# Performance work log

Hardware: AMD Instinct MI355X
Metric: run time of the kernel (lower is better)

Reference implementation:

```python
import jax, jax.numpy as jnp
from jax import lax
import numpy as np

# TopoLoss(dim=1, p=2, topo_lambda=1.0)
# p=2 -> Euclidean ground metric for the Vietoris-Rips filtration.
# This reference computes the dominant H0 persistence diagram of the VR complex:
# for a point cloud, H0 births are all 0 and deaths are exactly the MST edge
# weights (Kruskal/union-find == Prim, computed here with a fixed-length scan).
# Wasserstein distance between the two diagrams (equal cardinality N-1, births 0)
# reduces to optimal 1D matching of the sorted death values (q=1, the
# torch_topological WassersteinDistance default).
TOPO_LAMBDA = 1.0
EPS = 1e-12


def _pairwise_euclidean(x):
    # x: [B, N, D] -> [B, N, N] via the Gram trick (avoids [B,N,N,D] temp)
    sq = jnp.sum(x * x, axis=-1)                      # [B, N]
    g = jnp.einsum('bnd,bmd->bnm', x, x)              # [B, N, N]
    d2 = sq[:, :, None] + sq[:, None, :] - 2.0 * g
    return jnp.sqrt(jnp.maximum(d2, 0.0) + EPS)


def _mst_deaths(D):
    # Prim's algorithm on a dense distance matrix D: [N, N].
    # Returns the sorted MST edge weights = H0 death times ([N-1]).
    N = D.shape[0]
    inf = jnp.asarray(jnp.inf, D.dtype)
    in_tree0 = jnp.zeros((N,), bool).at[0].set(True)
    min_dist0 = D[0]

    def step(carry, _):
        in_tree, min_dist = carry
        masked = jnp.where(in_tree, inf, min_dist)
        j = jnp.argmin(masked)
        death = masked[j]
        in_tree = in_tree.at[j].set(True)
        min_dist = jnp.minimum(min_dist, D[j])
        return (in_tree, min_dist), death

    _, deaths = lax.scan(step, (in_tree0, min_dist0), None, length=N - 1)
    return jnp.sort(deaths)


def _h0_diagram_deaths(x):
    # x: [B, N, D] -> sorted death values [B, N-1]
    D = _pairwise_euclidean(x)
    return jax.vmap(_mst_deaths)(D)


def setup_inputs() -> dict:
    key = jax.random.key(0)
    k1, k2 = jax.random.split(key)
    B, N, D = 64, 1024, 3
    gts = jax.random.normal(k1, (B, N, D), dtype=jnp.float32)
    preds = jax.random.normal(k2, (B, N, D), dtype=jnp.float32)
    return {"gts": gts, "preds": preds}


def reference(gts, preds):
    # note: source names pers_info_pred = complex(gts) (vars swapped there);
    # Wasserstein is symmetric so ordering is irrelevant.
    deaths_a = _h0_diagram_deaths(gts)    # [B, N-1]
    deaths_b = _h0_diagram_deaths(preds)  # [B, N-1]
    # W1 between diagrams with equal cardinality and births==0:
    # optimal matching of sorted death coordinates.
    per_batch = jnp.sum(jnp.abs(deaths_a - deaths_b), axis=-1)  # [B]
    return per_batch.mean() * TOPO_LAMBDA
```

## Files before the change

### kernel.cpp

```cpp
#include <hip/hip_runtime.h>
#include <math.h>

#define N 1024
#define T 1024
#define HALF 512
#define PHASE_CAP 10
#define SWITCH 80

typedef float v2f __attribute__((ext_vector_type(2)));
typedef unsigned long long ull;

#define INF64 0xFFFFFFFFFFFFFFFFull
#define INF32 0xFFFFFFFFu

__device__ __forceinline__ unsigned umin32(unsigned a, unsigned b) { return a < b ? a : b; }
__device__ __forceinline__ unsigned umax32(unsigned a, unsigned b) { return a > b ? a : b; }
__device__ __forceinline__ int imin32(int a, int b) { return a < b ? a : b; }

__device__ __forceinline__ unsigned walk_root(const unsigned* parent, unsigned x) {
    unsigned prev = x, cur = parent[x];
    while (cur != prev) {
        unsigned nxt = parent[cur];
        if (nxt == prev) { cur = umin32(cur, prev); break; }
        prev = cur; cur = nxt;
    }
    return cur;
}

#define DPP_MIN_SHR(v, sh)                                                                   \
    do {                                                                                     \
        unsigned _t = (unsigned)__builtin_amdgcn_update_dpp(                                 \
            (int)0xFFFFFFFF, (int)(v), 0x110 | (sh), 0xF, 0xF, false);                       \
        (v) = umin32((v), _t);                                                               \
    } while (0)

__global__ __launch_bounds__(T) void scan1_kernel(const float* __restrict__ gts,
                                                  const float* __restrict__ preds,
                                                  unsigned* __restrict__ bests1) {
    __shared__ float px[N], py[N], pz[N];
    __shared__ float stage[3 * N];
    __shared__ unsigned pb[2][HALF];
    const int t = threadIdx.x;
    const int cloud = blockIdx.x >> 1;
    const int nh = blockIdx.x & 1;
    const float* __restrict__ src = (cloud < 64 ? gts : preds) + (size_t)(cloud & 63) * N * 3;

    if (t < 768) ((float4*)stage)[t] = ((const float4*)src)[t];
    __syncthreads();
    px[t] = stage[3 * t]; py[t] = stage[3 * t + 1]; pz[t] = stage[3 * t + 2];
    __syncthreads();

    const int node = nh * HALF + (t & (HALF - 1));
    const int jb = (t >> 9) * HALF;
    const float ax = px[node], ay = py[node], az = pz[node];
    const v2f axv = (v2f){ax, ax}, ayv = (v2f){ay, ay}, azv = (v2f){az, az};
    unsigned best = INF32;
    #pragma unroll 8
    for (int jj = 0; jj < HALF; jj += 2) {
        int j = jb + jj;
        v2f qx = *(const v2f*)&px[j];
        v2f qy = *(const v2f*)&py[j];
        v2f qz = *(const v2f*)&pz[j];
        v2f dx = axv - qx, dy = ayv - qy, dz = azv - qz;
        v2f e = dx * dx;
        e = __builtin_elementwise_fma(dy, dy, e);
        e = __builtin_elementwise_fma(dz, dz, e);
        unsigned k0 = (__float_as_uint(e.x) & 0xFFFFF800u) | (unsigned)j;
        unsigned k1 = (__float_as_uint(e.y) & 0xFFFFF800u) | (unsigned)(j + 1);
        k0 = (j == node) ? INF32 : k0;
        k1 = (j + 1 == node) ? INF32 : k1;
        best = umin32(best, umin32(k0, k1));
    }
    pb[t >> 9][t & (HALF - 1)] = best;
    __syncthreads();
    if (t < HALF)
        bests1[(size_t)cloud * N + nh * HALF + t] = umin32(pb[0][t], pb[1][t]);
}

__global__ __launch_bounds__(T) void scan2_kernel(const float* __restrict__ gts,
                                                  const float* __restrict__ preds,
                                                  const unsigned* __restrict__ bests1,
                                                  unsigned* __restrict__ bests2) {
    __shared__ float px[N], py[N], pz[N];
    __shared__ float stage[3 * N];
    __shared__ unsigned cw[N];
    __shared__ unsigned parent[N];
    __shared__ unsigned pb[2][HALF];
    const int t = threadIdx.x;
    const int cloud = blockIdx.x >> 1;
    const int nh = blockIdx.x & 1;
    const float* __restrict__ src = (cloud < 64 ? gts : preds) + (size_t)(cloud & 63) * N * 3;

    if (t < 768) ((float4*)stage)[t] = ((const float4*)src)[t];
    __syncthreads();
    px[t] = stage[3 * t]; py[t] = stage[3 * t + 1]; pz[t] = stage[3 * t + 2];
    parent[t] = bests1[(size_t)cloud * N + t] & 0x3FFu;
    __syncthreads();
    {
        unsigned r = walk_root(parent, (unsigned)t);
        parent[t] = r;
        cw[t] = r;
    }
    __syncthreads();

    const int node = nh * HALF + (t & (HALF - 1));
    const int jb = (t >> 9) * HALF;
    const unsigned c0 = cw[node];
    const float ax = px[node], ay = py[node], az = pz[node];
    const v2f axv = (v2f){ax, ax}, ayv = (v2f){ay, ay}, azv = (v2f){az, az};
    unsigned best = INF32;
    #pragma unroll 8
    for (int jj = 0; jj < HALF; jj += 2) {
        int j = jb + jj;
        v2f qx = *(const v2f*)&px[j];
        v2f qy = *(const v2f*)&py[j];
        v2f qz = *(const v2f*)&pz[j];
        uint2 cj = *(const uint2*)&cw[j];
        v2f dx = axv - qx, dy = ayv - qy, dz = azv - qz;
        v2f e = dx * dx;
        e = __builtin_elementwise_fma(dy, dy, e);
        e = __builtin_elementwise_fma(dz, dz, e);
        unsigned k0 = (__float_as_uint(e.x) & 0xFFFFF800u) | (unsigned)j;
        unsigned k1 = (__float_as_uint(e.y) & 0xFFFFF800u) | (unsigned)(j + 1);
        k0 = (cj.x == c0) ? INF32 : k0;
        k1 = (cj.y == c0) ? INF32 : k1;
        best = umin32(best, umin32(k0, k1));
    }
    pb[t >> 9][t & (HALF - 1)] = best;
    __syncthreads();
    if (t < HALF)
        bests2[(size_t)cloud * N + nh * HALF + t] = umin32(pb[0][t], pb[1][t]);
}

__global__ __launch_bounds__(T) void final_kernel(const float* __restrict__ gts,
                                                  const float* __restrict__ preds,
                                                  float* __restrict__ ws,
                                                  const unsigned* __restrict__ bests1,
                                                  const unsigned* __restrict__ bests2,
                                                  int nPre) {
    __shared__ float4 pts[N];
    __shared__ float4 spts[N];
    __shared__ unsigned comp[N];
    __shared__ ull bestComp[N];
    __shared__ unsigned parent[N];
    __shared__ __align__(16) unsigned pb[2][N];
    __shared__ float deaths[N];
    __shared__ unsigned wsum[16];
    __shared__ int deathCount;

    const int t = threadIdx.x;
    const int blk = blockIdx.x;
    const float* __restrict__ src = (blk < 64 ? gts : preds) + (size_t)(blk & 63) * N * 3;

    {
        float* stg = (float*)&spts[0];
        if (t < 768) ((float4*)stg)[t] = ((const float4*)src)[t];
        __syncthreads();
        float x = stg[3 * t], y = stg[3 * t + 1], z = stg[3 * t + 2];
        pts[t] = make_float4(x, y, z, __uint_as_float((unsigned)t));
        comp[t] = (unsigned)t;
        parent[t] = (unsigned)t;
        deaths[t] = 0.0f;
        bestComp[t] = INF64;
    }
    if (t == 0) deathCount = 0;
    __syncthreads();

    const int n = t & (HALF - 1);
    const int h = t >> 9;
    const int n2 = n + HALF;
    const int jbase = h * HALF;
    float4 pA = pts[n], pB = pts[n2];
    const v2f pxv = (v2f){pA.x, pB.x};
    const v2f pyv = (v2f){pA.y, pB.y};
    const v2f pzv = (v2f){pA.z, pB.z};

    if (nPre >= 1) {
        unsigned b1 = bests1[(size_t)blk * N + t];
        unsigned j1 = b1 & 0x3FFu;
        unsigned e1 = b1 & 0xFFFFF800u;
        parent[t] = j1;
        __syncthreads();
        {
            unsigned p = j1;
            unsigned gp = parent[p];
            bool mutual = (gp == (unsigned)t);
            bool rec = !mutual || ((unsigned)t < p);
            float dval = rec ? sqrtf(__uint_as_float(e1) + 1e-12f) : 0.0f;
            ull m = __ballot(rec);
            int cnt = __popcll(m);
            int base = 0;
            if ((t & 63) == 0 && cnt) base = atomicAdd(&deathCount, cnt);
            base = __shfl(base, 0, 64);
            if (rec) {
                int idx = base + __popcll(m & ((1ull << (t & 63)) - 1ull));
                if (idx < N - 1) deaths[idx] = dval;
            }
        }
        __syncthreads();
        {
            unsigned r = walk_root(parent, (unsigned)t);
            parent[t] = r;
            comp[t] = r;
            pts[t].w = __uint_as_float(r);
        }
        __syncthreads();
    }

    if (nPre >= 2) {
        unsigned b2 = bests2[(size_t)blk * N + t];
        if (b2 != INF32) {
            unsigned j2 = b2 & 0x3FFu, e2 = b2 & 0xFFFFF800u;
            unsigned mn = umin32((unsigned)t, j2), mx = umax32((unsigned)t, j2);
            atomicMin(&bestComp[comp[t]], ((ull)e2 << 20) | (ull)((mn << 10) | mx));
        }
        __syncthreads();
        const unsigned c = (unsigned)t;
        const bool isRoot = (parent[c] == c);
        {
            ull bc = bestComp[c];
            if (isRoot && bc != INF64) {
                unsigned mn = (unsigned)((bc >> 10) & 0x3FFu);
                unsigned mx = (unsigned)(bc & 0x3FFu);
                unsigned cm = comp[mn];
                parent[c] = (cm == c) ? comp[mx] : cm;
            }
        }
        __syncthreads();
        {
            bool rec = false;
            float dval = 0.0f;
            unsigned p = parent[c];
            if (isRoot && p != c) {
                unsigned gp = parent[p];
                bool mutual = (gp == c);
                rec = !mutual || (c < p);
                if (rec) dval = sqrtf(__uint_as_float((unsigned)(bestComp[c] >> 20)) + 1e-12f);
            }
            ull m = __ballot(rec);
            int cnt = __popcll(m);
            int base = 0;
            if ((t & 63) == 0 && cnt) base = atomicAdd(&deathCount, cnt);
            base = __shfl(base, 0, 64);
            if (rec) {
                int idx = base + __popcll(m & ((1ull << (t & 63)) - 1ull));
                if (idx < N - 1) deaths[idx] = dval;
            }
        }
        __syncthreads();
        {
            unsigned r = walk_root(parent, c);
            parent[t] = r;
            unsigned nc = walk_root(parent, comp[t]);
            comp[t] = nc;
            pts[t].w = __uint_as_float(nc);
            bestComp[t] = INF64;
        }
        __syncthreads();
    }

    int phase = nPre;
    while (N - deathCount > SWITCH && phase < PHASE_CAP) {
        const unsigned c0 = comp[n], c1 = comp[n2];
        unsigned best0 = INF32, best1 = INF32;
        #pragma unroll 8
        for (int jj = 0; jj < HALF; ++jj) {
            int j = jbase + jj;
            float4 pj = pts[j];
            unsigned cj = __float_as_uint(pj.w);
            v2f dx = pxv - (v2f){pj.x, pj.x};
            v2f dy = pyv - (v2f){pj.y, pj.y};
            v2f dz = pzv - (v2f){pj.z, pj.z};
            v2f e = dx * dx;
            e = __builtin_elementwise_fma(dy, dy, e);
            e = __builtin_elementwise_fma(dz, dz, e);
            unsigned k0 = (__float_as_uint(e.x) & 0xFFFFF800u) | (unsigned)j;
            unsigned k1 = (__float_as_uint(e.y) & 0xFFFFF800u) | (unsigned)j;
            k0 = (cj == c0) ? INF32 : k0;
            k1 = (cj == c1) ? INF32 : k1;
            best0 = umin32(best0, k0);
            best1 = umin32(best1, k1);
        }
        pb[h][n] = best0;
        pb[h][n2] = best1;
        __syncthreads();
        if (h == 0) {
            #pragma unroll
            for (int s = 0; s < 2; ++s) {
                int m = s == 0 ? n : n2;
                unsigned fb = umin32(pb[0][m], pb[1][m]);
                if (fb != INF32) {
                    unsigned j = fb & 0x3FFu, e = fb & 0xFFFFF800u;
                    unsigned mn = umin32((unsigned)m, j), mx = umax32((unsigned)m, j);
                    ull key = ((ull)e << 20) | (ull)((mn << 10) | mx);
                    if (phase == 0) bestComp[m] = key;
                    else atomicMin(&bestComp[comp[m]], key);
                }
            }
        }
        __syncthreads();
        const unsigned c = (unsigned)t;
        const bool isRoot = (parent[c] == c);
        {
            ull bc = bestComp[c];
            if (isRoot && bc != INF64) {
                unsigned mn = (unsigned)((bc >> 10) & 0x3FFu);
                unsigned mx = (unsigned)(bc & 0x3FFu);
                unsigned cm = comp[mn];
                parent[c] = (cm == c) ? comp[mx] : cm;
            }
        }
        __syncthreads();
        {
            bool rec = false;
            float dval = 0.0f;
            unsigned p = parent[c];
            if (isRoot && p != c) {
                unsigned gp = parent[p];
                bool mutual = (gp == c);
                rec = !mutual || (c < p);
                if (rec) dval = sqrtf(__uint_as_float((unsigned)(bestComp[c] >> 20)) + 1e-12f);
            }
            ull m = __ballot(rec);
            int cnt = __popcll(m);
            int base = 0;
            if ((t & 63) == 0 && cnt) base = atomicAdd(&deathCount, cnt);
            base = __shfl(base, 0, 64);
            if (rec) {
                int idx = base + __popcll(m & ((1ull << (t & 63)) - 1ull));
                if (idx < N - 1) deaths[idx] = dval;
            }
        }
        __syncthreads();
        {
            unsigned r = walk_root(parent, c);
            parent[t] = r;
            unsigned nc = walk_root(parent, comp[t]);
            comp[t] = nc;
            pts[t].w = __uint_as_float(nc);
            bestComp[t] = INF64;
        }
        __syncthreads();
        ++phase;
    }

    const int dcbase = deathCount;
    const int comps = N - dcbase;
    if (comps > 1) {
        unsigned* scomp = &pb[0][0];
        unsigned* hist = &pb[1][0];
        unsigned* wavemin = &pb[1][0];
        uint2* segs = (uint2*)&bestComp[0];
        const int lane = t & 63;
        const int wid = t >> 6;

        hist[t] = 0;
        __syncthreads();
        atomicAdd(&hist[comp[t]], 1u);
        __syncthreads();
        unsigned cnt = hist[t];
        unsigned inc = cnt;
        #pragma unroll
        for (int d = 1; d < 64; d <<= 1) {
            unsigned u = __shfl_up(inc, d, 64);
            if (lane >= d) inc += u;
        }
        if (lane == 63) wsum[wid] = inc;
        __syncthreads();
        unsigned wof = 0;
        for (int i = 0; i < wid; ++i) wof += wsum[i];
        unsigned excl = wof + inc - cnt;
        if (cnt) { segs[t].x = excl; segs[t].y = excl + cnt; }
        __syncthreads();
        hist[t] = excl;
        __syncthreads();
        {
            unsigned pos = atomicAdd(&hist[comp[t]], 1u);
            spts[pos] = pts[t];
            scomp[pos] = comp[t];
        }
        __syncthreads();

        unsigned c_cur = comp[0];
        v2f pxv2 = (v2f){0.f, 0.f}, pyv2 = pxv2, pzv2 = pxv2;
        unsigned myc0 = 0, myc1 = 0, md0 = INF32, md1 = INF32;
        if (t < HALF) {
            float4 q0 = spts[t], q1 = spts[t + HALF];
            myc0 = scomp[t];
            myc1 = scomp[t + HALF];
            pxv2 = (v2f){q0.x, q1.x};
            pyv2 = (v2f){q0.y, q1.y};
            pzv2 = (v2f){q0.z, q1.z};
            if (myc0 == c_cur) pxv2.x = INFINITY;
            if (myc1 == c_cur) pxv2.y = INFINITY;
        }

        for (int step = 0; step < comps - 1; ++step) {
            if (t < HALF) {
                uint2 sg = segs[c_cur];
                const int jb = (int)sg.x, je = (int)sg.y, jl = je - 1;
                for (int base = jb; base < je; base += 4) {
                    float4 q0 = spts[base];
                    float4 q1 = spts[imin32(base + 1, jl)];
                    float4 q2 = spts[imin32(base + 2, jl)];
                    float4 q3 = spts[imin32(base + 3, jl)];
                    #define RELAX(qq)                                                        \
                        {                                                                    \
                            v2f dx = pxv2 - (v2f){qq.x, qq.x};                               \
                            v2f dy = pyv2 - (v2f){qq.y, qq.y};                               \
                            v2f dz = pzv2 - (v2f){qq.z, qq.z};                               \
                            v2f e = dx * dx;                                                 \
                            e = __builtin_elementwise_fma(dy, dy, e);                        \
                            e = __builtin_elementwise_fma(dz, dz, e);                        \
                            md0 = umin32(md0, (__float_as_uint(e.x) & 0xFFFFFC00u) | myc0);  \
                            md1 = umin32(md1, (__float_as_uint(e.y) & 0xFFFFFC00u) | myc1);  \
                        }
                    RELAX(q0) RELAX(q1) RELAX(q2) RELAX(q3)
                    #undef RELAX
                }
                unsigned v = umin32(md0, md1);
                DPP_MIN_SHR(v, 1);
                DPP_MIN_SHR(v, 2);
                DPP_MIN_SHR(v, 4);
                DPP_MIN_SHR(v, 8);
                unsigned r0 = (unsigned)__builtin_amdgcn_readlane((int)v, 15);
                unsigned r1 = (unsigned)__builtin_amdgcn_readlane((int)v, 31);
                unsigned r2 = (unsigned)__builtin_amdgcn_readlane((int)v, 47);
                unsigned r3 = (unsigned)__builtin_amdgcn_readlane((int)v, 63);
                if (lane == 0)
                    wavemin[(step & 1) * 8 + wid] = umin32(umin32(r0, r1), umin32(r2, r3));
            }
            __syncthreads();
            if (t < HALF) {
                const uint4* wmv = (const uint4*)(wavemin + (step & 1) * 8);
                uint4 u0 = wmv[0], u1 = wmv[1];
                unsigned m0 = umin32(umin32(u0.x, u0.y), umin32(u0.z, u0.w));
                unsigned m1 = umin32(umin32(u1.x, u1.y), umin32(u1.z, u1.w));
                unsigned G = umin32(m0, m1);
                c_cur = G & 0x3FFu;
                if (t == 0)
                    deaths[dcbase + step] = sqrtf(__uint_as_float(G & 0xFFFFFC00u) + 1e-12f);
                if (myc0 == c_cur) { pxv2.x = INFINITY; md0 = INF32; }
                if (myc1 == c_cur) { pxv2.y = INFINITY; md1 = INF32; }
            }
        }
    }

    if (t == 0) deaths[N - 1] = INFINITY;
    __syncthreads();
    {
        float v = deaths[t];
        #pragma unroll
        for (int k = 2; k <= N; k <<= 1) {
            const bool up = ((t & k) == 0);
            #pragma unroll
            for (int j = k >> 1; j > 0; j >>= 1) {
                float u;
                if (j >= 64) {
                    deaths[t] = v;
                    __syncthreads();
                    u = deaths[t ^ j];
                    __syncthreads();
                } else {
                    u = __shfl_xor(v, j, 64);
                }
                v = (((t & j) == 0) == up) ? fminf(v, u) : fmaxf(v, u);
            }
        }
        float* dst = ws + (size_t)blk * N;
        dst[t] = (t < N - 1) ? v : 0.0f;
    }
}

__global__ __launch_bounds__(256) void diff_kernel(const float* __restrict__ ws,
                                                   float* __restrict__ out) {
    __shared__ float red[4];
    const int t = threadIdx.x;
    const int b = blockIdx.x;
    const float* a = ws + (size_t)b * N;
    const float* c = ws + (size_t)(64 + b) * N;
    float sum = 0.0f;
    for (int i = t; i < N; i += 256)
        sum += fabsf(a[i] - c[i]);
    #pragma unroll
    for (int off = 32; off > 0; off >>= 1)
        sum += __shfl_down(sum, off, 64);
    if ((t & 63) == 0) red[t >> 6] = sum;
    __syncthreads();
    if (t == 0)
        atomicAdd(out, (red[0] + red[1] + red[2] + red[3]) * (1.0f / 64.0f));
}

extern "C" void kernel_launch(void* const* d_in, const int* in_sizes, int n_in,
                              void* d_out, int out_size, void* d_ws, size_t ws_size,
                              hipStream_t stream) {
    const float* gts = (const float*)d_in[0];
    const float* preds = (const float*)d_in[1];
    float* ws = (float*)d_ws;
    unsigned* bests1 = (unsigned*)d_ws;
    unsigned* bests2 = bests1 + 128 * N;
    const bool big = ws_size >= (size_t)(2u * 128u * N * 4u);

    if (big) {
        hipLaunchKernelGGL(scan1_kernel, dim3(256), dim3(T), 0, stream, gts, preds, bests1);
        hipLaunchKernelGGL(scan2_kernel, dim3(256), dim3(T), 0, stream, gts, preds, bests1, bests2);
        hipLaunchKernelGGL(final_kernel, dim3(128), dim3(T), 0, stream,
                           gts, preds, ws, bests1, bests2, 2);
    } else {
        hipLaunchKernelGGL(final_kernel, dim3(128), dim3(T), 0, stream,
                           gts, preds, ws, (const unsigned*)nullptr, (const unsigned*)nullptr, 0);
    }
    hipMemsetAsync(d_out, 0, sizeof(float), stream);
    hipLaunchKernelGGL(diff_kernel, dim3(64), dim3(256), 0, stream, ws, (float*)d_out);
}
```

Measured before the change: 223.3 us.

## Register-block four query nodes per thread in Boruvka scan kernels

Each thread in scan1 and scan2 now handles four query nodes packed into two v2f registers and sweeps a 128-candidate slice, instead of one node over 512 candidates. Every candidate point loaded from LDS is reused against four nodes, cutting shared-memory loads per distance, and the partial minima are reduced across eight slices instead of two. In exchange it uses more registers and a slightly larger final reduction.

```diff
diff --git a/kernel.cpp b/kernel.cpp
--- a/kernel.cpp
+++ b/kernel.cpp
@@ -39,7 +39,7 @@
                                                   unsigned* __restrict__ bests1) {
     __shared__ float px[N], py[N], pz[N];
     __shared__ float stage[3 * N];
-    __shared__ unsigned pb[2][HALF];
+    __shared__ unsigned pb8[8][HALF];
     const int t = threadIdx.x;
     const int cloud = blockIdx.x >> 1;
     const int nh = blockIdx.x & 1;
@@ -50,31 +50,52 @@
     px[t] = stage[3 * t]; py[t] = stage[3 * t + 1]; pz[t] = stage[3 * t + 2];
     __syncthreads();
 
-    const int node = nh * HALF + (t & (HALF - 1));
-    const int jb = (t >> 9) * HALF;
-    const float ax = px[node], ay = py[node], az = pz[node];
-    const v2f axv = (v2f){ax, ax}, ayv = (v2f){ay, ay}, azv = (v2f){az, az};
-    unsigned best = INF32;
-    #pragma unroll 8
-    for (int jj = 0; jj < HALF; jj += 2) {
-        int j = jb + jj;
+    const int q = t & 127;
+    const int s = t >> 7;
+    const int jbase = s << 7;
+    const int n0 = nh * HALF + q;
+    const int n1 = n0 + 128, n2 = n0 + 256, n3 = n0 + 384;
+    const v2f axA = (v2f){px[n0], px[n1]}, ayA = (v2f){py[n0], py[n1]}, azA = (v2f){pz[n0], pz[n1]};
+    const v2f axB = (v2f){px[n2], px[n3]}, ayB = (v2f){py[n2], py[n3]}, azB = (v2f){pz[n2], pz[n3]};
+    unsigned b0 = INF32, b1 = INF32, b2 = INF32, b3 = INF32;
+    #pragma unroll 4
+    for (int jj = 0; jj < 128; jj += 2) {
+        const int j = jbase + jj;
         v2f qx = *(const v2f*)&px[j];
         v2f qy = *(const v2f*)&py[j];
         v2f qz = *(const v2f*)&pz[j];
-        v2f dx = axv - qx, dy = ayv - qy, dz = azv - qz;
-        v2f e = dx * dx;
-        e = __builtin_elementwise_fma(dy, dy, e);
-        e = __builtin_elementwise_fma(dz, dz, e);
-        unsigned k0 = (__float_as_uint(e.x) & 0xFFFFF800u) | (unsigned)j;
-        unsigned k1 = (__float_as_uint(e.y) & 0xFFFFF800u) | (unsigned)(j + 1);
-        k0 = (j == node) ? INF32 : k0;
-        k1 = (j + 1 == node) ? INF32 : k1;
-        best = umin32(best, umin32(k0, k1));
-    }
-    pb[t >> 9][t & (HALF - 1)] = best;
-    __syncthreads();
-    if (t < HALF)
-        bests1[(size_t)cloud * N + nh * HALF + t] = umin32(pb[0][t], pb[1][t]);
+        #define STEP1(SX, SY, SZ, JV)                                                   \
+        {                                                                               \
+            const v2f sxv = (v2f){SX, SX}, syv = (v2f){SY, SY}, szv = (v2f){SZ, SZ};    \
+            v2f dxA = axA - sxv, dyA = ayA - syv, dzA = azA - szv;                      \
+            v2f eA = dxA * dxA;                                                         \
+            eA = __builtin_elementwise_fma(dyA, dyA, eA);                               \
+            eA = __builtin_elementwise_fma(dzA, dzA, eA);                               \
+            v2f dxB = axB - sxv, dyB = ayB - syv, dzB = azB - szv;                      \
+            v2f eB = dxB * dxB;                                                         \
+            eB = __builtin_elementwise_fma(dyB, dyB, eB);                               \
+            eB = __builtin_elementwise_fma(dzB, dzB, eB);                               \
+            unsigned kk;                                                                \
+            kk = (__float_as_uint(eA.x) & 0xFFFFF800u) | (unsigned)(JV);                \
+            b0 = umin32(b0, ((JV) == n0) ? INF32 : kk);                                 \
+            kk = (__float_as_uint(eA.y) & 0xFFFFF800u) | (unsigned)(JV);                \
+            b1 = umin32(b1, ((JV) == n1) ? INF32 : kk);                                 \
+            kk = (__float_as_uint(eB.x) & 0xFFFFF800u) | (unsigned)(JV);                \
+            b2 = umin32(b2, ((JV) == n2) ? INF32 : kk);                                 \
+            kk = (__float_as_uint(eB.y) & 0xFFFFF800u) | (unsigned)(JV);                \
+            b3 = umin32(b3, ((JV) == n3) ? INF32 : kk);                                 \
+        }
+        STEP1(qx.x, qy.x, qz.x, j)
+        STEP1(qx.y, qy.y, qz.y, j + 1)
+        #undef STEP1
+    }
+    pb8[s][q] = b0; pb8[s][q + 128] = b1; pb8[s][q + 256] = b2; pb8[s][q + 384] = b3;
+    __syncthreads();
+    if (t < HALF) {
+        unsigned best = umin32(umin32(pb8[0][t], pb8[1][t]), umin32(pb8[2][t], pb8[3][t]));
+        best = umin32(best, umin32(umin32(pb8[4][t], pb8[5][t]), umin32(pb8[6][t], pb8[7][t])));
+        bests1[(size_t)cloud * N + nh * HALF + t] = best;
+    }
 }
 
 __global__ __launch_bounds__(T) void scan2_kernel(const float* __restrict__ gts,
@@ -85,7 +106,7 @@
     __shared__ float stage[3 * N];
     __shared__ unsigned cw[N];
     __shared__ unsigned parent[N];
-    __shared__ unsigned pb[2][HALF];
+    __shared__ unsigned pb8[8][HALF];
     const int t = threadIdx.x;
     const int cloud = blockIdx.x >> 1;
     const int nh = blockIdx.x & 1;
@@ -103,33 +124,54 @@
     }
     __syncthreads();
 
-    const int node = nh * HALF + (t & (HALF - 1));
-    const int jb = (t >> 9) * HALF;
-    const unsigned c0 = cw[node];
-    const float ax = px[node], ay = py[node], az = pz[node];
-    const v2f axv = (v2f){ax, ax}, ayv = (v2f){ay, ay}, azv = (v2f){az, az};
-    unsigned best = INF32;
-    #pragma unroll 8
-    for (int jj = 0; jj < HALF; jj += 2) {
-        int j = jb + jj;
+    const int q = t & 127;
+    const int s = t >> 7;
+    const int jbase = s << 7;
+    const int n0 = nh * HALF + q;
+    const int n1 = n0 + 128, n2 = n0 + 256, n3 = n0 + 384;
+    const unsigned c0 = cw[n0], c1 = cw[n1], c2 = cw[n2], c3 = cw[n3];
+    const v2f axA = (v2f){px[n0], px[n1]}, ayA = (v2f){py[n0], py[n1]}, azA = (v2f){pz[n0], pz[n1]};
+    const v2f axB = (v2f){px[n2], px[n3]}, ayB = (v2f){py[n2], py[n3]}, azB = (v2f){pz[n2], pz[n3]};
+    unsigned b0 = INF32, b1 = INF32, b2 = INF32, b3 = INF32;
+    #pragma unroll 4
+    for (int jj = 0; jj < 128; jj += 2) {
+        const int j = jbase + jj;
         v2f qx = *(const v2f*)&px[j];
         v2f qy = *(const v2f*)&py[j];
         v2f qz = *(const v2f*)&pz[j];
         uint2 cj = *(const uint2*)&cw[j];
-        v2f dx = axv - qx, dy = ayv - qy, dz = azv - qz;
-        v2f e = dx * dx;
-        e = __builtin_elementwise_fma(dy, dy, e);
-        e = __builtin_elementwise_fma(dz, dz, e);
-        unsigned k0 = (__float_as_uint(e.x) & 0xFFFFF800u) | (unsigned)j;
-        unsigned k1 = (__float_as_uint(e.y) & 0xFFFFF800u) | (unsigned)(j + 1);
-        k0 = (cj.x == c0) ? INF32 : k0;
-        k1 = (cj.y == c0) ? INF32 : k1;
-        best = umin32(best, umin32(k0, k1));
-    }
-    pb[t >> 9][t & (HALF - 1)] = best;
-    __syncthreads();
-    if (t < HALF)
-        bests2[(size_t)cloud * N + nh * HALF + t] = umin32(pb[0][t], pb[1][t]);
+        #define STEP2(SX, SY, SZ, CJ, JV)                                               \
+        {                                                                               \
+            const v2f sxv = (v2f){SX, SX}, syv = (v2f){SY, SY}, szv = (v2f){SZ, SZ};    \
+            v2f dxA = axA - sxv, dyA = ayA - syv, dzA = azA - szv;                      \
+            v2f eA = dxA * dxA;                                                         \
+            eA = __builtin_elementwise_fma(dyA, dyA, eA);                               \
+            eA = __builtin_elementwise_fma(dzA, dzA, eA);                               \
+            v2f dxB = axB - sxv, dyB = ayB - syv, dzB = azB - szv;                      \
+            v2f eB = dxB * dxB;                                                         \
+            eB = __builtin_elementwise_fma(dyB, dyB, eB);                               \
+            eB = __builtin_elementwise_fma(dzB, dzB, eB);                               \
+            unsigned kk;                                                                \
+            kk = (__float_as_uint(eA.x) & 0xFFFFF800u) | (unsigned)(JV);                \
+            b0 = umin32(b0, ((CJ) == c0) ? INF32 : kk);                                 \
+            kk = (__float_as_uint(eA.y) & 0xFFFFF800u) | (unsigned)(JV);                \
+            b1 = umin32(b1, ((CJ) == c1) ? INF32 : kk);                                 \
+            kk = (__float_as_uint(eB.x) & 0xFFFFF800u) | (unsigned)(JV);                \
+            b2 = umin32(b2, ((CJ) == c2) ? INF32 : kk);                                 \
+            kk = (__float_as_uint(eB.y) & 0xFFFFF800u) | (unsigned)(JV);                \
+            b3 = umin32(b3, ((CJ) == c3) ? INF32 : kk);                                 \
+        }
+        STEP2(qx.x, qy.x, qz.x, cj.x, j)
+        STEP2(qx.y, qy.y, qz.y, cj.y, j + 1)
+        #undef STEP2
+    }
+    pb8[s][q] = b0; pb8[s][q + 128] = b1; pb8[s][q + 256] = b2; pb8[s][q + 384] = b3;
+    __syncthreads();
+    if (t < HALF) {
+        unsigned best = umin32(umin32(pb8[0][t], pb8[1][t]), umin32(pb8[2][t], pb8[3][t]));
+        best = umin32(best, umin32(umin32(pb8[4][t], pb8[5][t]), umin32(pb8[6][t], pb8[7][t])));
+        bests2[(size_t)cloud * N + nh * HALF + t] = best;
+    }
 }
 
 __global__ __launch_bounds__(T) void final_kernel(const float* __restrict__ gts,
```

Result: no change. 219.4 us (-1.7%).

## Fuse scan passes, Boruvka phases and final reduction into one mega kernel

Applied to the files above, without the earlier changes.

Replaces the separate scan1, scan2 and final kernels with a single per-cloud mega_kernel. The two nearest-neighbour scan passes are done in shared memory by one 1024-thread block per cloud instead of being split over two blocks through global workspace. The diff stage appears to be folded in with a ticket counter, so the last block writes the output. This removes launch overhead and global round trips, but halves the number of blocks doing the scan work, which costs parallelism in the heavy first phases.

```diff
diff --git a/kernel.cpp b/kernel.cpp
--- a/kernel.cpp
+++ b/kernel.cpp
@@ -34,110 +34,452 @@
         (v) = umin32((v), _t);                                                               \
     } while (0)
 
-__global__ __launch_bounds__(T) void scan1_kernel(const float* __restrict__ gts,
-                                                  const float* __restrict__ preds,
-                                                  unsigned* __restrict__ bests1) {
-    __shared__ float px[N], py[N], pz[N];
-    __shared__ float stage[3 * N];
-    __shared__ unsigned pb[2][HALF];
+struct MegaSmem {
+    float4 pts[N];
+    float deaths[N];
+    ull bestComp[N];
+    unsigned comp[N];
+    unsigned pb[2][N];
+    union {
+        struct {
+            unsigned pb4hi[2][N];
+            unsigned bests[N];
+            unsigned parent[N];
+        } a;
+        float4 spts[N];
+        float stage[3 * N];
+    } u;
+    unsigned wsum[16];
+    int deathCount;
+    int ticket;
+    float red4[2][4][4];
+};
+
+template <bool SUPP_COMP>
+__device__ __forceinline__ void scan_pass(MegaSmem& S, int t) {
+    const int q = t & 255;
+    const int s = t >> 8;
+    const int jbase = s << 8;
+    const int n0 = q, n1 = q + 256, n2 = q + 512, n3 = q + 768;
+    const float4 p0 = S.pts[n0], p1 = S.pts[n1], p2 = S.pts[n2], p3 = S.pts[n3];
+    const v2f axA = (v2f){p0.x, p1.x}, ayA = (v2f){p0.y, p1.y}, azA = (v2f){p0.z, p1.z};
+    const v2f axB = (v2f){p2.x, p3.x}, ayB = (v2f){p2.y, p3.y}, azB = (v2f){p2.z, p3.z};
+    unsigned c0 = 0, c1 = 0, c2 = 0, c3 = 0;
+    if (SUPP_COMP) { c0 = S.comp[n0]; c1 = S.comp[n1]; c2 = S.comp[n2]; c3 = S.comp[n3]; }
+    unsigned b0 = INF32, b1 = INF32, b2 = INF32, b3 = INF32;
+    #pragma unroll 4
+    for (int jj = 0; jj < 256; jj += 2) {
+        const int j = jbase + jj;
+        const float4 qa = S.pts[j];
+        const float4 qb = S.pts[j + 1];
+        uint2 cj;
+        if (SUPP_COMP) cj = *(const uint2*)&S.comp[j];
+        #define MSTEP(QQ, CJV, JV)                                                       \
+        {                                                                                \
+            const v2f sxv = (v2f){QQ.x, QQ.x}, syv = (v2f){QQ.y, QQ.y},                  \
+                      szv = (v2f){QQ.z, QQ.z};                                           \
+            v2f dxA = axA - sxv, dyA = ayA - syv, dzA = azA - szv;                       \
+            v2f eA = dxA * dxA;                                                          \
+            eA = __builtin_elementwise_fma(dyA, dyA, eA);                                \
+            eA = __builtin_elementwise_fma(dzA, dzA, eA);                                \
+            v2f dxB = axB - sxv, dyB = ayB - syv, dzB = azB - szv;                       \
+            v2f eB = dxB * dxB;                                                          \
+            eB = __builtin_elementwise_fma(dyB, dyB, eB);                                \
+            eB = __builtin_elementwise_fma(dzB, dzB, eB);                                \
+            unsigned kk;                                                                 \
+            kk = (__float_as_uint(eA.x) & 0xFFFFF800u) | (unsigned)(JV);                 \
+            b0 = umin32(b0, (SUPP_COMP ? ((CJV) == c0) : ((JV) == n0)) ? INF32 : kk);    \
+            kk = (__float_as_uint(eA.y) & 0xFFFFF800u) | (unsigned)(JV);                 \
+            b1 = umin32(b1, (SUPP_COMP ? ((CJV) == c1) : ((JV) == n1)) ? INF32 : kk);    \
+            kk = (__float_as_uint(eB.x) & 0xFFFFF800u) | (unsigned)(JV);                 \
+            b2 = umin32(b2, (SUPP_COMP ? ((CJV) == c2) : ((JV) == n2)) ? INF32 : kk);    \
+            kk = (__float_as_uint(eB.y) & 0xFFFFF800u) | (unsigned)(JV);                 \
+            b3 = umin32(b3, (SUPP_COMP ? ((CJV) == c3) : ((JV) == n3)) ? INF32 : kk);    \
+        }
+        MSTEP(qa, cj.x, j)
+        MSTEP(qb, cj.y, j + 1)
+        #undef MSTEP
+    }
+    unsigned* prow = (s < 2) ? &S.pb[s][0] : &S.u.a.pb4hi[s - 2][0];
+    prow[n0] = b0; prow[n1] = b1; prow[n2] = b2; prow[n3] = b3;
+    __syncthreads();
+    {
+        unsigned best = umin32(umin32(S.pb[0][t], S.pb[1][t]),
+                               umin32(S.u.a.pb4hi[0][t], S.u.a.pb4hi[1][t]));
+        S.u.a.bests[t] = best;
+    }
+    __syncthreads();
+}
+
+__global__ __launch_bounds__(T) void mega_kernel(const float* __restrict__ gts,
+                                                 const float* __restrict__ preds,
+                                                 float* __restrict__ ws,
+                                                 float* __restrict__ out,
+                                                 unsigned* __restrict__ ctr) {
+    __shared__ MegaSmem S;
     const int t = threadIdx.x;
-    const int cloud = blockIdx.x >> 1;
-    const int nh = blockIdx.x & 1;
-    const float* __restrict__ src = (cloud < 64 ? gts : preds) + (size_t)(cloud & 63) * N * 3;
-
-    if (t < 768) ((float4*)stage)[t] = ((const float4*)src)[t];
-    __syncthreads();
-    px[t] = stage[3 * t]; py[t] = stage[3 * t + 1]; pz[t] = stage[3 * t + 2];
-    __syncthreads();
-
-    const int node = nh * HALF + (t & (HALF - 1));
-    const int jb = (t >> 9) * HALF;
-    const float ax = px[node], ay = py[node], az = pz[node];
-    const v2f axv = (v2f){ax, ax}, ayv = (v2f){ay, ay}, azv = (v2f){az, az};
-    unsigned best = INF32;
-    #pragma unroll 8
-    for (int jj = 0; jj < HALF; jj += 2) {
-        int j = jb + jj;
-        v2f qx = *(const v2f*)&px[j];
-        v2f qy = *(const v2f*)&py[j];
-        v2f qz = *(const v2f*)&pz[j];
-        v2f dx = axv - qx, dy = ayv - qy, dz = azv - qz;
-        v2f e = dx * dx;
-        e = __builtin_elementwise_fma(dy, dy, e);
-        e = __builtin_elementwise_fma(dz, dz, e);
-        unsigned k0 = (__float_as_uint(e.x) & 0xFFFFF800u) | (unsigned)j;
-        unsigned k1 = (__float_as_uint(e.y) & 0xFFFFF800u) | (unsigned)(j + 1);
-        k0 = (j == node) ? INF32 : k0;
-        k1 = (j + 1 == node) ? INF32 : k1;
-        best = umin32(best, umin32(k0, k1));
-    }
-    pb[t >> 9][t & (HALF - 1)] = best;
-    __syncthreads();
-    if (t < HALF)
-        bests1[(size_t)cloud * N + nh * HALF + t] = umin32(pb[0][t], pb[1][t]);
-}
-
-__global__ __launch_bounds__(T) void scan2_kernel(const float* __restrict__ gts,
-                                                  const float* __restrict__ preds,
-                                                  const unsigned* __restrict__ bests1,
-                                                  unsigned* __restrict__ bests2) {
-    __shared__ float px[N], py[N], pz[N];
-    __shared__ float stage[3 * N];
-    __shared__ unsigned cw[N];
-    __shared__ unsigned parent[N];
-    __shared__ unsigned pb[2][HALF];
-    const int t = threadIdx.x;
-    const int cloud = blockIdx.x >> 1;
-    const int nh = blockIdx.x & 1;
-    const float* __restrict__ src = (cloud < 64 ? gts : preds) + (size_t)(cloud & 63) * N * 3;
-
-    if (t < 768) ((float4*)stage)[t] = ((const float4*)src)[t];
-    __syncthreads();
-    px[t] = stage[3 * t]; py[t] = stage[3 * t + 1]; pz[t] = stage[3 * t + 2];
-    parent[t] = bests1[(size_t)cloud * N + t] & 0x3FFu;
-    __syncthreads();
-    {
-        unsigned r = walk_root(parent, (unsigned)t);
-        parent[t] = r;
-        cw[t] = r;
-    }
-    __syncthreads();
-
-    const int node = nh * HALF + (t & (HALF - 1));
-    const int jb = (t >> 9) * HALF;
-    const unsigned c0 = cw[node];
-    const float ax = px[node], ay = py[node], az = pz[node];
-    const v2f axv = (v2f){ax, ax}, ayv = (v2f){ay, ay}, azv = (v2f){az, az};
-    unsigned best = INF32;
-    #pragma unroll 8
-    for (int jj = 0; jj < HALF; jj += 2) {
-        int j = jb + jj;
-        v2f qx = *(const v2f*)&px[j];
-        v2f qy = *(const v2f*)&py[j];
-        v2f qz = *(const v2f*)&pz[j];
-        uint2 cj = *(const uint2*)&cw[j];
-        v2f dx = axv - qx, dy = ayv - qy, dz = azv - qz;
-        v2f e = dx * dx;
-        e = __builtin_elementwise_fma(dy, dy, e);
-        e = __builtin_elementwise_fma(dz, dz, e);
-        unsigned k0 = (__float_as_uint(e.x) & 0xFFFFF800u) | (unsigned)j;
-        unsigned k1 = (__float_as_uint(e.y) & 0xFFFFF800u) | (unsigned)(j + 1);
-        k0 = (cj.x == c0) ? INF32 : k0;
-        k1 = (cj.y == c0) ? INF32 : k1;
-        best = umin32(best, umin32(k0, k1));
-    }
-    pb[t >> 9][t & (HALF - 1)] = best;
-    __syncthreads();
-    if (t < HALF)
-        bests2[(size_t)cloud * N + nh * HALF + t] = umin32(pb[0][t], pb[1][t]);
+    const int blk = blockIdx.x;
+    const float* __restrict__ src = (blk < 64 ? gts : preds) + (size_t)(blk & 63) * N * 3;
+
+    if (t < 768) ((float4*)S.u.stage)[t] = ((const float4*)src)[t];
+    __syncthreads();
+    {
+        const float x = S.u.stage[3 * t], y = S.u.stage[3 * t + 1], z = S.u.stage[3 * t + 2];
+        __syncthreads();
+        S.pts[t] = make_float4(x, y, z, __uint_as_float((unsigned)t));
+        S.comp[t] = (unsigned)t;
+        S.u.a.parent[t] = (unsigned)t;
+        S.deaths[t] = 0.0f;
+        S.bestComp[t] = INF64;
+        if (t == 0) S.deathCount = 0;
+    }
+    __syncthreads();
+
+    scan_pass<false>(S, t);
+
+    {
+        unsigned b1v = S.u.a.bests[t];
+        unsigned j1 = b1v & 0x3FFu;
+        unsigned e1 = b1v & 0xFFFFF800u;
+        S.u.a.parent[t] = j1;
+        __syncthreads();
+        {
+            unsigned p = j1;
+            unsigned gp = S.u.a.parent[p];
+            bool mutual = (gp == (unsigned)t);
+            bool rec = !mutual || ((unsigned)t < p);
+            float dval = rec ? sqrtf(__uint_as_float(e1) + 1e-12f) : 0.0f;
+            ull m = __ballot(rec);
+            int cnt = __popcll(m);
+            int base = 0;
+            if ((t & 63) == 0 && cnt) base = atomicAdd(&S.deathCount, cnt);
+            base = __shfl(base, 0, 64);
+            if (rec) {
+                int idx = base + __popcll(m & ((1ull << (t & 63)) - 1ull));
+                if (idx < N - 1) S.deaths[idx] = dval;
+            }
+        }
+        __syncthreads();
+        {
+            unsigned r = walk_root(S.u.a.parent, (unsigned)t);
+            S.u.a.parent[t] = r;
+            S.comp[t] = r;
+            S.pts[t].w = __uint_as_float(r);
+        }
+        __syncthreads();
+    }
+
+    scan_pass<true>(S, t);
+
+    {
+        unsigned b2v = S.u.a.bests[t];
+        if (b2v != INF32) {
+            unsigned j2 = b2v & 0x3FFu, e2 = b2v & 0xFFFFF800u;
+            unsigned mn = umin32((unsigned)t, j2), mx = umax32((unsigned)t, j2);
+            atomicMin(&S.bestComp[S.comp[t]], ((ull)e2 << 20) | (ull)((mn << 10) | mx));
+        }
+        __syncthreads();
+        const unsigned c = (unsigned)t;
+        const bool isRoot = (S.u.a.parent[c] == c);
+        {
+            ull bc = S.bestComp[c];
+            if (isRoot && bc != INF64) {
+                unsigned mn = (unsigned)((bc >> 10) & 0x3FFu);
+                unsigned mx = (unsigned)(bc & 0x3FFu);
+                unsigned cm = S.comp[mn];
+                S.u.a.parent[c] = (cm == c) ? S.comp[mx] : cm;
+            }
+        }
+        __syncthreads();
+        {
+            bool rec = false;
+            float dval = 0.0f;
+            unsigned p = S.u.a.parent[c];
+            if (isRoot && p != c) {
+                unsigned gp = S.u.a.parent[p];
+                bool mutual = (gp == c);
+                rec = !mutual || (c < p);
+                if (rec) dval = sqrtf(__uint_as_float((unsigned)(S.bestComp[c] >> 20)) + 1e-12f);
+            }
+            ull m = __ballot(rec);
+            int cnt = __popcll(m);
+            int base = 0;
+            if ((t & 63) == 0 && cnt) base = atomicAdd(&S.deathCount, cnt);
+            base = __shfl(base, 0, 64);
+            if (rec) {
+                int idx = base + __popcll(m & ((1ull << (t & 63)) - 1ull));
+                if (idx < N - 1) S.deaths[idx] = dval;
+            }
+        }
+        __syncthreads();
+        {
+            unsigned r = walk_root(S.u.a.parent, c);
+            S.u.a.parent[t] = r;
+            unsigned nc = walk_root(S.u.a.parent, S.comp[t]);
+            S.comp[t] = nc;
+            S.pts[t].w = __uint_as_float(nc);
+            S.bestComp[t] = INF64;
+        }
+        __syncthreads();
+    }
+
+    {
+        const int n = t & (HALF - 1);
+        const int h = t >> 9;
+        const int n2 = n + HALF;
+        const int jb2 = h * HALF;
+        float4 pA = S.pts[n], pB = S.pts[n2];
+        const v2f pxv = (v2f){pA.x, pB.x};
+        const v2f pyv = (v2f){pA.y, pB.y};
+        const v2f pzv = (v2f){pA.z, pB.z};
+        int phase = 2;
+        while (N - S.deathCount > SWITCH && phase < PHASE_CAP) {
+            const unsigned c0 = S.comp[n], c1 = S.comp[n2];
+            unsigned best0 = INF32, best1 = INF32;
+            #pragma unroll 8
+            for (int jj = 0; jj < HALF; ++jj) {
+                int j = jb2 + jj;
+                float4 pj = S.pts[j];
+                unsigned cj = __float_as_uint(pj.w);
+                v2f dx = pxv - (v2f){pj.x, pj.x};
+                v2f dy = pyv - (v2f){pj.y, pj.y};
+                v2f dz = pzv - (v2f){pj.z, pj.z};
+                v2f e = dx * dx;
+                e = __builtin_elementwise_fma(dy, dy, e);
+                e = __builtin_elementwise_fma(dz, dz, e);
+                unsigned k0 = (__float_as_uint(e.x) & 0xFFFFF800u) | (unsigned)j;
+                unsigned k1 = (__float_as_uint(e.y) & 0xFFFFF800u) | (unsigned)j;
+                k0 = (cj == c0) ? INF32 : k0;
+                k1 = (cj == c1) ? INF32 : k1;
+                best0 = umin32(best0, k0);
+                best1 = umin32(best1, k1);
+            }
+            S.pb[h][n] = best0;
+            S.pb[h][n2] = best1;
+            __syncthreads();
+            if (h == 0) {
+                #pragma unroll
+                for (int sS = 0; sS < 2; ++sS) {
+                    int m = sS == 0 ? n : n2;
+                    unsigned fb = umin32(S.pb[0][m], S.pb[1][m]);
+                    if (fb != INF32) {
+                        unsigned j = fb & 0x3FFu, e = fb & 0xFFFFF800u;
+                        unsigned mn = umin32((unsigned)m, j), mx = umax32((unsigned)m, j);
+                        ull key = ((ull)e << 20) | (ull)((mn << 10) | mx);
+                        atomicMin(&S.bestComp[S.comp[m]], key);
+                    }
+                }
+            }
+            __syncthreads();
+            const unsigned c = (unsigned)t;
+            const bool isRoot = (S.u.a.parent[c] == c);
+            {
+                ull bc = S.bestComp[c];
+                if (isRoot && bc != INF64) {
+                    unsigned mn = (unsigned)((bc >> 10) & 0x3FFu);
+                    unsigned mx = (unsigned)(bc & 0x3FFu);
+                    unsigned cm = S.comp[mn];
+                    S.u.a.parent[c] = (cm == c) ? S.comp[mx] : cm;
+                }
+            }
+            __syncthreads();
+            {
+                bool rec = false;
+                float dval = 0.0f;
+                unsigned p = S.u.a.parent[c];
+                if (isRoot && p != c) {
+                    unsigned gp = S.u.a.parent[p];
+                    bool mutual = (gp == c);
+                    rec = !mutual || (c < p);
+                    if (rec)
+                        dval = sqrtf(__uint_as_float((unsigned)(S.bestComp[c] >> 20)) + 1e-12f);
+                }
+                ull m = __ballot(rec);
+                int cnt = __popcll(m);
+                int base = 0;
+                if ((t & 63) == 0 && cnt) base = atomicAdd(&S.deathCount, cnt);
+                base = __shfl(base, 0, 64);
+                if (rec) {
+                    int idx = base + __popcll(m & ((1ull << (t & 63)) - 1ull));
+                    if (idx < N - 1) S.deaths[idx] = dval;
+                }
+            }
+            __syncthreads();
+            {
+                unsigned r = walk_root(S.u.a.parent, c);
+                S.u.a.parent[t] = r;
+                unsigned nc = walk_root(S.u.a.parent, S.comp[t]);
+                S.comp[t] = nc;
+                S.pts[t].w = __uint_as_float(nc);
+                S.bestComp[t] = INF64;
+            }
+            __syncthreads();
+            ++phase;
+        }
+    }
+
+    const int dcbase = S.deathCount;
+    const int comps = N - dcbase;
+    if (comps > 1) {
+        unsigned* scomp = &S.pb[0][0];
+        unsigned* hist = &S.pb[1][0];
+        unsigned* wavemin = &S.pb[1][0];
+        uint2* segs = (uint2*)&S.bestComp[0];
+        const int lane = t & 63;
+        const int wid = t >> 6;
+
+        hist[t] = 0;
+        __syncthreads();
+        atomicAdd(&hist[S.comp[t]], 1u);
+        __syncthreads();
+        unsigned cnt = hist[t];
+        unsigned inc = cnt;
+        #pragma unroll
+        for (int d = 1; d < 64; d <<= 1) {
+            unsigned uu = __shfl_up(inc, d, 64);
+            if (lane >= d) inc += uu;
+        }
+        if (lane == 63) S.wsum[wid] = inc;
+        __syncthreads();
+        unsigned wof = 0;
+        for (int i = 0; i < wid; ++i) wof += S.wsum[i];
+        unsigned excl = wof + inc - cnt;
+        if (cnt) { segs[t].x = excl; segs[t].y = excl + cnt; }
+        __syncthreads();
+        hist[t] = excl;
+        __syncthreads();
+        {
+            unsigned pos = atomicAdd(&hist[S.comp[t]], 1u);
+            S.u.spts[pos] = S.pts[t];
+            scomp[pos] = S.comp[t];
+        }
+        __syncthreads();
+
+        unsigned c_cur = S.comp[0];
+        v2f pxv2 = (v2f){0.f, 0.f}, pyv2 = pxv2, pzv2 = pxv2;
+        unsigned myc0 = 0, myc1 = 0, md0 = INF32, md1 = INF32;
+        if (t < HALF) {
+            float4 q0 = S.u.spts[t], q1 = S.u.spts[t + HALF];
+            myc0 = scomp[t];
+            myc1 = scomp[t + HALF];
+            pxv2 = (v2f){q0.x, q1.x};
+            pyv2 = (v2f){q0.y, q1.y};
+            pzv2 = (v2f){q0.z, q1.z};
+            if (myc0 == c_cur) pxv2.x = INFINITY;
+            if (myc1 == c_cur) pxv2.y = INFINITY;
+        }
+
+        for (int step = 0; step < comps - 1; ++step) {
+            if (t < HALF) {
+                uint2 sg = segs[c_cur];
+                const int jb = (int)sg.x, je = (int)sg.y, jl = je - 1;
+                for (int base = jb; base < je; base += 4) {
+                    float4 q0 = S.u.spts[base];
+                    float4 q1 = S.u.spts[imin32(base + 1, jl)];
+                    float4 q2 = S.u.spts[imin32(base + 2, jl)];
+                    float4 q3 = S.u.spts[imin32(base + 3, jl)];
+                    #define RELAX(qq)                                                        \
+                        {                                                                    \
+                            v2f dx = pxv2 - (v2f){qq.x, qq.x};                               \
+                            v2f dy = pyv2 - (v2f){qq.y, qq.y};                               \
+                            v2f dz = pzv2 - (v2f){qq.z, qq.z};                               \
+                            v2f e = dx * dx;                                                 \
+                            e = __builtin_elementwise_fma(dy, dy, e);                        \
+                            e = __builtin_elementwise_fma(dz, dz, e);                        \
+                            md0 = umin32(md0, (__float_as_uint(e.x) & 0xFFFFFC00u) | myc0);  \
+                            md1 = umin32(md1, (__float_as_uint(e.y) & 0xFFFFFC00u) | myc1);  \
+                        }
+                    RELAX(q0) RELAX(q1) RELAX(q2) RELAX(q3)
+                    #undef RELAX
+                }
+                unsigned v = umin32(md0, md1);
+                DPP_MIN_SHR(v, 1);
+                DPP_MIN_SHR(v, 2);
+                DPP_MIN_SHR(v, 4);
+                DPP_MIN_SHR(v, 8);
+                unsigned r0 = (unsigned)__builtin_amdgcn_readlane((int)v, 15);
+                unsigned r1 = (unsigned)__builtin_amdgcn_readlane((int)v, 31);
+                unsigned r2 = (unsigned)__builtin_amdgcn_readlane((int)v, 47);
+                unsigned r3 = (unsigned)__builtin_amdgcn_readlane((int)v, 63);
+                if (lane == 0)
+                    wavemin[(step & 1) * 8 + wid] = umin32(umin32(r0, r1), umin32(r2, r3));
+            }
+            __syncthreads();
+            if (t < HALF) {
+                const uint4* wmv = (const uint4*)(wavemin + (step & 1) * 8);
+                uint4 u0 = wmv[0], u1 = wmv[1];
+                unsigned m0 = umin32(umin32(u0.x, u0.y), umin32(u0.z, u0.w));
+                unsigned m1 = umin32(umin32(u1.x, u1.y), umin32(u1.z, u1.w));
+                unsigned G = umin32(m0, m1);
+                c_cur = G & 0x3FFu;
+                if (t == 0)
+                    S.deaths[dcbase + step] = sqrtf(__uint_as_float(G & 0xFFFFFC00u) + 1e-12f);
+                if (myc0 == c_cur) { pxv2.x = INFINITY; md0 = INF32; }
+                if (myc1 == c_cur) { pxv2.y = INFINITY; md1 = INF32; }
+            }
+        }
+    }
+
+    if (t == 0) S.deaths[N - 1] = INFINITY;
+    __syncthreads();
+    {
+        float v = S.deaths[t];
+        #pragma unroll
+        for (int k = 2; k <= N; k <<= 1) {
+            const bool up = ((t & k) == 0);
+            #pragma unroll
+            for (int j = k >> 1; j > 0; j >>= 1) {
+                float uu;
+                if (j >= 64) {
+                    S.deaths[t] = v;
+                    __syncthreads();
+                    uu = S.deaths[t ^ j];
+                    __syncthreads();
+                } else {
+                    uu = __shfl_xor(v, j, 64);
+                }
+                v = (((t & j) == 0) == up) ? fminf(v, uu) : fmaxf(v, uu);
+            }
+        }
+        float* dst = ws + (size_t)blk * N;
+        dst[t] = (t < N - 1) ? v : 0.0f;
+    }
+
+    __threadfence();
+    __syncthreads();
+    if (t == 0) S.ticket = (int)atomicAdd(ctr, 1u);
+    __syncthreads();
+    if (S.ticket == 127) {
+        __threadfence();
+        const int g = t >> 8, tl = t & 255;
+        float acc = 0.0f;
+        for (int chunk = 0; chunk < 16; ++chunk) {
+            const int b = (chunk << 2) + g;
+            const float* a = ws + (size_t)b * N;
+            const float* c = ws + (size_t)(64 + b) * N;
+            float sum = 0.0f;
+            for (int i = tl; i < N; i += 256)
+                sum += fabsf(a[i] - c[i]);
+            #pragma unroll
+            for (int off = 32; off > 0; off >>= 1)
+                sum += __shfl_down(sum, off, 64);
+            if ((tl & 63) == 0) S.red4[chunk & 1][g][tl >> 6] = sum;
+            __syncthreads();
+            if (t == 0) {
+                #pragma unroll
+                for (int gg = 0; gg < 4; ++gg) {
+                    const float* r = S.red4[chunk & 1][gg];
+                    acc += (r[0] + r[1] + r[2] + r[3]) * (1.0f / 64.0f);
+                }
+            }
+        }
+        if (t == 0) out[0] = acc;
+    }
 }
 
 __global__ __launch_bounds__(T) void final_kernel(const float* __restrict__ gts,
                                                   const float* __restrict__ preds,
-                                                  float* __restrict__ ws,
-                                                  const unsigned* __restrict__ bests1,
-                                                  const unsigned* __restrict__ bests2,
-                                                  int nPre) {
+                                                  float* __restrict__ ws) {
     __shared__ float4 pts[N];
     __shared__ float4 spts[N];
     __shared__ unsigned comp[N];
@@ -175,92 +517,8 @@
     const v2f pyv = (v2f){pA.y, pB.y};
     const v2f pzv = (v2f){pA.z, pB.z};
 
-    if (nPre >= 1) {
-        unsigned b1 = bests1[(size_t)blk * N + t];
-        unsigned j1 = b1 & 0x3FFu;
-        unsigned e1 = b1 & 0xFFFFF800u;
-        parent[t] = j1;
-        __syncthreads();
-        {
-            unsigned p = j1;
-            unsigned gp = parent[p];
-            bool mutual = (gp == (unsigned)t);
-            bool rec = !mutual || ((unsigned)t < p);
-            float dval = rec ? sqrtf(__uint_as_float(e1) + 1e-12f) : 0.0f;
-            ull m = __ballot(rec);
-            int cnt = __popcll(m);
-            int base = 0;
-            if ((t & 63) == 0 && cnt) base = atomicAdd(&deathCount, cnt);
-            base = __shfl(base, 0, 64);
-            if (rec) {
-                int idx = base + __popcll(m & ((1ull << (t & 63)) - 1ull));
-                if (idx < N - 1) deaths[idx] = dval;
-            }
-        }
-        __syncthreads();
-        {
-            unsigned r = walk_root(parent, (unsigned)t);
-            parent[t] = r;
-            comp[t] = r;
-            pts[t].w = __uint_as_float(r);
-        }
-        __syncthreads();
-    }
-
-    if (nPre >= 2) {
-        unsigned b2 = bests2[(size_t)blk * N + t];
-        if (b2 != INF32) {
-            unsigned j2 = b2 & 0x3FFu, e2 = b2 & 0xFFFFF800u;
-            unsigned mn = umin32((unsigned)t, j2), mx = umax32((unsigned)t, j2);
-            atomicMin(&bestComp[comp[t]], ((ull)e2 << 20) | (ull)((mn << 10) | mx));
-        }
-        __syncthreads();
-        const unsigned c = (unsigned)t;
-        const bool isRoot = (parent[c] == c);
-        {
-            ull bc = bestComp[c];
-            if (isRoot && bc != INF64) {
-                unsigned mn = (unsigned)((bc >> 10) & 0x3FFu);
-                unsigned mx = (unsigned)(bc & 0x3FFu);
-                unsigned cm = comp[mn];
-                parent[c] = (cm == c) ? comp[mx] : cm;
-            }
-        }
-        __syncthreads();
-        {
-            bool rec = false;
-            float dval = 0.0f;
-            unsigned p = parent[c];
-            if (isRoot && p != c) {
-                unsigned gp = parent[p];
-                bool mutual = (gp == c);
-                rec = !mutual || (c < p);
-                if (rec) dval = sqrtf(__uint_as_float((unsigned)(bestComp[c] >> 20)) + 1e-12f);
-            }
-            ull m = __ballot(rec);
-            int cnt = __popcll(m);
-            int base = 0;
-            if ((t & 63) == 0 && cnt) base = atomicAdd(&deathCount, cnt);
-            base = __shfl(base, 0, 64);
-            if (rec) {
-                int idx = base + __popcll(m & ((1ull << (t & 63)) - 1ull));
-                if (idx < N - 1) deaths[idx] = dval;
-            }
-        }
-        __syncthreads();
-        {
-            unsigned r = walk_root(parent, c);
-            parent[t] = r;
-            unsigned nc = walk_root(parent, comp[t]);
-            comp[t] = nc;
-            pts[t].w = __uint_as_float(nc);
-            bestComp[t] = INF64;
-        }
-        __syncthreads();
-    }
-
-    int phase = nPre;
-    while (N - deathCount > SWITCH && phase < PHASE_CAP) {
+    int phase = 0;
+    while (N - deathCount > 1 && phase < PHASE_CAP) {
         const unsigned c0 = comp[n], c1 = comp[n2];
         unsigned best0 = INF32, best1 = INF32;
         #pragma unroll 8
@@ -344,108 +602,6 @@
         ++phase;
     }
 
-    const int dcbase = deathCount;
-    const int comps = N - dcbase;
-    if (comps > 1) {
-        unsigned* scomp = &pb[0][0];
-        unsigned* hist = &pb[1][0];
-        unsigned* wavemin = &pb[1][0];
-        uint2* segs = (uint2*)&bestComp[0];
-        const int lane = t & 63;
-        const int wid = t >> 6;
-
-        hist[t] = 0;
-        __syncthreads();
-        atomicAdd(&hist[comp[t]], 1u);
-        __syncthreads();
-        unsigned cnt = hist[t];
-        unsigned inc = cnt;
-        #pragma unroll
-        for (int d = 1; d < 64; d <<= 1) {
-            unsigned u = __shfl_up(inc, d, 64);
-            if (lane >= d) inc += u;
-        }
-        if (lane == 63) wsum[wid] = inc;
-        __syncthreads();
-        unsigned wof = 0;
-        for (int i = 0; i < wid; ++i) wof += wsum[i];
-        unsigned excl = wof + inc - cnt;
-        if (cnt) { segs[t].x = excl; segs[t].y = excl + cnt; }
-        __syncthreads();
-        hist[t] = excl;
-        __syncthreads();
-        {
-            unsigned pos = atomicAdd(&hist[comp[t]], 1u);
-            spts[pos] = pts[t];
-            scomp[pos] = comp[t];
-        }
-        __syncthreads();
-
-        unsigned c_cur = comp[0];
-        v2f pxv2 = (v2f){0.f, 0.f}, pyv2 = pxv2, pzv2 = pxv2;
-        unsigned myc0 = 0, myc1 = 0, md0 = INF32, md1 = INF32;
-        if (t < HALF) {
-            float4 q0 = spts[t], q1 = spts[t + HALF];
-            myc0 = scomp[t];
-            myc1 = scomp[t + HALF];
-            pxv2 = (v2f){q0.x, q1.x};
-            pyv2 = (v2f){q0.y, q1.y};
-            pzv2 = (v2f){q0.z, q1.z};
-            if (myc0 == c_cur) pxv2.x = INFINITY;
-            if (myc1 == c_cur) pxv2.y = INFINITY;
-        }
-
-        for (int step = 0; step < comps - 1; ++step) {
-            if (t < HALF) {
-                uint2 sg = segs[c_cur];
-                const int jb = (int)sg.x, je = (int)sg.y, jl = je - 1;
-                for (int base = jb; base < je; base += 4) {
-                    float4 q0 = spts[base];
-                    float4 q1 = spts[imin32(base + 1, jl)];
-                    float4 q2 = spts[imin32(base + 2, jl)];
-                    float4 q3 = spts[imin32(base + 3, jl)];
-                    #define RELAX(qq)                                                        \
-                        {                                                                    \
-                            v2f dx = pxv2 - (v2f){qq.x, qq.x};                               \
-                            v2f dy = pyv2 - (v2f){qq.y, qq.y};                               \
-                            v2f dz = pzv2 - (v2f){qq.z, qq.z};                               \
-                            v2f e = dx * dx;                                                 \
-                            e = __builtin_elementwise_fma(dy, dy, e);                        \
-                            e = __builtin_elementwise_fma(dz, dz, e);                        \
-                            md0 = umin32(md0, (__float_as_uint(e.x) & 0xFFFFFC00u) | myc0);  \
-                            md1 = umin32(md1, (__float_as_uint(e.y) & 0xFFFFFC00u) | myc1);  \
-                        }
-                    RELAX(q0) RELAX(q1) RELAX(q2) RELAX(q3)
-                    #undef RELAX
-                }
-                unsigned v = umin32(md0, md1);
-                DPP_MIN_SHR(v, 1);
-                DPP_MIN_SHR(v, 2);
-                DPP_MIN_SHR(v, 4);
-                DPP_MIN_SHR(v, 8);
-                unsigned r0 = (unsigned)__builtin_amdgcn_readlane((int)v, 15);
-                unsigned r1 = (unsigned)__builtin_amdgcn_readlane((int)v, 31);
-                unsigned r2 = (unsigned)__builtin_amdgcn_readlane((int)v, 47);
-                unsigned r3 = (unsigned)__builtin_amdgcn_readlane((int)v, 63);
-                if (lane == 0)
-                    wavemin[(step & 1) * 8 + wid] = umin32(umin32(r0, r1), umin32(r2, r3));
-            }
-            __syncthreads();
-            if (t < HALF) {
-                const uint4* wmv = (const uint4*)(wavemin + (step & 1) * 8);
-                uint4 u0 = wmv[0], u1 = wmv[1];
-                unsigned m0 = umin32(umin32(u0.x, u0.y), umin32(u0.z, u0.w));
-                unsigned m1 = umin32(umin32(u1.x, u1.y), umin32(u1.z, u1.w));
-                unsigned G = umin32(m0, m1);
-                c_cur = G & 0x3FFu;
-                if (t == 0)
-                    deaths[dcbase + step] = sqrtf(__uint_as_float(G & 0xFFFFFC00u) + 1e-12f);
-                if (myc0 == c_cur) { pxv2.x = INFINITY; md0 = INF32; }
-                if (myc1 == c_cur) { pxv2.y = INFINITY; md1 = INF32; }
-            }
-        }
-    }
-
     if (t == 0) deaths[N - 1] = INFINITY;
     __syncthreads();
     {
@@ -497,19 +653,16 @@
     const float* gts = (const float*)d_in[0];
     const float* preds = (const float*)d_in[1];
     float* ws = (float*)d_ws;
-    unsigned* bests1 = (unsigned*)d_ws;
-    unsigned* bests2 = bests1 + 128 * N;
     const bool big = ws_size >= (size_t)(2u * 128u * N * 4u);
 
     if (big) {
-        hipLaunchKernelGGL(scan1_kernel, dim3(256), dim3(T), 0, stream, gts, preds, bests1);
-        hipLaunchKernelGGL(scan2_kernel, dim3(256), dim3(T), 0, stream, gts, preds, bests1, bests2);
-        hipLaunchKernelGGL(final_kernel, dim3(128), dim3(T), 0, stream,
-                           gts, preds, ws, bests1, bests2, 2);
+        unsigned* ctr = (unsigned*)(ws + (size_t)128 * N);
+        hipMemsetAsync(ctr, 0, sizeof(unsigned), stream);
+        hipLaunchKernelGGL(mega_kernel, dim3(128), dim3(T), 0, stream,
+                           gts, preds, ws, (float*)d_out, ctr);
     } else {
-        hipLaunchKernelGGL(final_kernel, dim3(128), dim3(T), 0, stream,
-                           gts, preds, ws, (const unsigned*)nullptr, (const unsigned*)nullptr, 0);
-    }
-    hipMemsetAsync(d_out, 0, sizeof(float), stream);
-    hipLaunchKernelGGL(diff_kernel, dim3(64), dim3(256), 0, stream, ws, (float*)d_out);
+        hipLaunchKernelGGL(final_kernel, dim3(128), dim3(T), 0, stream, gts, preds, ws);
+        hipMemsetAsync(d_out, 0, sizeof(float), stream);
+        hipLaunchKernelGGL(diff_kernel, dim3(64), dim3(256), 0, stream, ws, (float*)d_out);
+    }
 }
```

New measurement: 323.9 us. 1.45x slower.
